# Kernel optimization log

Hardware: AMD Instinct MI355X
Metric: run time of the kernel (lower is better)

## Reference

```python
import jax, jax.numpy as jnp
import numpy as np

OUT = 7                # adaptive pool output size (7,7)
SPATIAL_SCALE = 1.0 / 16.0
NEG = jnp.float32(-3.0e38)  # acts as -inf for masked max


def setup_inputs() -> dict:
    key = jax.random.key(0)
    k1, k2, k3, k4, k5, k6 = jax.random.split(key, 6)
    B, C, H, W = 2, 256, 50, 50
    R = 256
    features = jax.random.normal(k1, (B, C, H, W), dtype=jnp.float32)
    # boxes in image coordinates (image = 800x800, stride 16)
    x1 = jax.random.uniform(k2, (R,), minval=0.0, maxval=500.0)
    y1 = jax.random.uniform(k3, (R,), minval=0.0, maxval=500.0)
    bw = jax.random.uniform(k4, (R,), minval=64.0, maxval=296.0)
    bh = jax.random.uniform(k5, (R,), minval=64.0, maxval=296.0)
    rois = jnp.stack([x1, y1, x1 + bw, y1 + bh], axis=1).astype(jnp.float32)  # [R,4]
    roi_indices = jax.random.randint(k6, (R,), 0, B, dtype=jnp.int64)
    return {"features": features, "rois": rois, "roi_indices": roi_indices}


def _roi_pool(features, rois, roi_indices):
    H, W = features.shape[2], features.shape[3]
    ri = (rois * SPATIAL_SCALE).astype(jnp.int32)           # truncation, as np.astype
    x1, y1, x2, y2 = ri[:, 0], ri[:, 1], ri[:, 2], ri[:, 3]
    # NOTE: original code slices features[idx, :, x1:x2, y1:y2] -> x indexes dim H, y indexes dim W
    Lh = x2 - x1                                            # [R]
    Lw = y2 - y1
    p = jnp.arange(OUT)
    # adaptive max pool bin boundaries (torch semantics): start=floor(i*L/OUT), end=ceil((i+1)*L/OUT)
    hstart = x1[:, None] + (p[None, :] * Lh[:, None]) // OUT                   # [R,OUT]
    hend = x1[:, None] + ((p[None, :] + 1) * Lh[:, None] + OUT - 1) // OUT
    wstart = y1[:, None] + (p[None, :] * Lw[:, None]) // OUT
    wend = y1[:, None] + ((p[None, :] + 1) * Lw[:, None] + OUT - 1) // OUT
    hidx = jnp.arange(H)
    widx = jnp.arange(W)
    row_mask = (hidx[None, None, :] >= hstart[:, :, None]) & (hidx[None, None, :] < hend[:, :, None])  # [R,OUT,H]
    col_mask = (widx[None, None, :] >= wstart[:, :, None]) & (widx[None, None, :] < wend[:, :, None])  # [R,OUT,W]

    feat = features[roi_indices]                            # [R,C,H,W]
    # reduce over W per output column (fixed small loop over OUT bins)
    cols = []
    for pw in range(OUT):
        m = col_mask[:, pw][:, None, None, :]               # [R,1,1,W]
        cols.append(jnp.max(jnp.where(m, feat, NEG), axis=3))  # [R,C,H]
    t = jnp.stack(cols, axis=-1)                            # [R,C,H,OUT]
    # reduce over H per output row
    rows = []
    for ph in range(OUT):
        m = row_mask[:, ph][:, None, :, None]               # [R,1,H,1]
        rows.append(jnp.max(jnp.where(m, t, NEG), axis=2))  # [R,C,OUT]
    return jnp.stack(rows, axis=2)                          # [R,C,OUT,OUT]


def reference(features, rois, roi_indices):
    return _roi_pool(features, rois, roi_indices)
```

## Files before the change

### kernel.cpp

```cpp
#include <hip/hip_runtime.h>
#include <cstddef>


namespace {
constexpr int OUTP = 7;
constexpr int CC = 256;
constexpr int HH = 50;
constexpr int WW = 50;
constexpr int HWSZ = HH * WW;
constexpr int CSPLIT = 8;
constexpr int CPS = CC / CSPLIT;
constexpr float NEGV = -3e38f;
constexpr int LMAX = 19;
constexpr int RSTR = 21;
constexpr int CSTR = LMAX * RSTR;
typedef float vf4 __attribute__((ext_vector_type(4), aligned(4)));
}

__global__ __launch_bounds__(256, 3) void roipool_fused(
    const float* __restrict__ feat, const float* __restrict__ rois,
    const int* __restrict__ ridx, float* __restrict__ out) {
    __shared__ float buf[CPS * CSTR];

    const int s = blockIdx.x;
    const int r = blockIdx.y;
    const int tid = threadIdx.x;

    const float4 rv = reinterpret_cast<const float4*>(rois)[r];
    int x1 = (int)(rv.x * 0.0625f);
    int y1 = (int)(rv.y * 0.0625f);
    int x2 = (int)(rv.z * 0.0625f);
    int y2 = (int)(rv.w * 0.0625f);
    int b = ridx[r];
    x1 = __builtin_amdgcn_readfirstlane(x1);
    y1 = __builtin_amdgcn_readfirstlane(y1);
    x2 = __builtin_amdgcn_readfirstlane(x2);
    y2 = __builtin_amdgcn_readfirstlane(y2);
    b = __builtin_amdgcn_readfirstlane(b);

    const int Lh = x2 - x1;
    const int Lw = y2 - y1;

    const float* fb = feat + (size_t)(b * CC + s * CPS) * HWSZ;
    float* obase = out + (size_t)(r * CC + s * CPS) * (OUTP * OUTP);

    const bool fast = (Lh >= 1 && Lh <= LMAX && Lw >= 1 && Lw <= LMAX &&
                       x1 >= 0 && y1 >= 0 && x2 < HH && y2 < WW);

    if (fast) {
        {
            const int c = tid >> 3;
            const int j = tid & 7;
            if (j < 5) {
                const float* gp = fb + (size_t)c * HWSZ + (size_t)x1 * WW + y1 + j * 4;
                float* lp = buf + c * CSTR + j * 4;
                for (int row = 0; row < Lh; ++row) {
                    const vf4 v = *reinterpret_cast<const vf4*>(gp + row * WW);
                    float* q = lp + row * RSTR;
                    q[0] = v.x;
                    q[1] = v.y;
                    q[2] = v.z;
                    q[3] = v.w;
                }
            }
        }
        __syncthreads();

        const int cc = tid & 31;
        const int q = tid >> 5;
        const float* cb = buf + cc * CSTR;
        float* ob = obase + (size_t)cc * (OUTP * OUTP);

#pragma unroll
        for (int k = 0; k < 7; ++k) {
            const int bin = q + k * 8;
            if (bin < 49) {
                const int ph = bin / OUTP;
                const int pw = bin - ph * OUTP;
                const int h0 = (ph * Lh) / OUTP;
                const int nh = ((ph + 1) * Lh + OUTP - 1) / OUTP - h0;
                const int w0 = (pw * Lw) / OUTP;
                const int nw = ((pw + 1) * Lw + OUTP - 1) / OUTP - w0;
                const float* wb = cb + h0 * RSTR + w0;
                float m = NEGV;
#pragma unroll
                for (int i = 0; i < 4; ++i) {
                    const int ro = (i < nh ? i : nh - 1) * RSTR;
#pragma unroll
                    for (int jj = 0; jj < 4; ++jj) {
                        const int co = (jj < nw ? jj : nw - 1);
                        m = fmaxf(m, wb[ro + co]);
                    }
                }
                __builtin_nontemporal_store(m, ob + bin);
            }
        }
    } else {
        const int cc = tid & 31;
        const int q = tid >> 5;
        const float* cb = fb + (size_t)cc * HWSZ;
        float* ob = obase + (size_t)cc * (OUTP * OUTP);

        for (int k = 0; k < 7; ++k) {
            const int bin = q + k * 8;
            if (bin < 49) {
                const int ph = bin / OUTP;
                const int pw = bin - ph * OUTP;
                int hs = x1 + (ph * Lh) / OUTP;
                int he = x1 + ((ph + 1) * Lh + OUTP - 1) / OUTP;
                int ws = y1 + (pw * Lw) / OUTP;
                int we = y1 + ((pw + 1) * Lw + OUTP - 1) / OUTP;
                hs = hs < 0 ? 0 : hs;
                he = he > HH ? HH : he;
                ws = ws < 0 ? 0 : ws;
                we = we > WW ? WW : we;
                float m = NEGV;
                for (int h = hs; h < he; ++h) {
                    for (int w = ws; w < we; ++w) {
                        m = fmaxf(m, cb[h * WW + w]);
                    }
                }
                ob[bin] = m;
            }
        }
    }
}

extern "C" void kernel_launch(void* const* d_in, const int* in_sizes, int n_in,
                              void* d_out, int out_size, void* d_ws, size_t ws_size,
                              hipStream_t stream) {
    const float* features = (const float*)d_in[0];
    const float* rois = (const float*)d_in[1];
    const int* ridx = (const int*)d_in[2];
    float* out = (float*)d_out;
    const int R = in_sizes[1] / 4;

    roipool_fused<<<dim3(CSPLIT, R), 256, 0, stream>>>(features, rois, ridx, out);
}
```

Baseline: 24.01 us.

## Split channels finer and stage ROI via aligned float2 loads spread over all threads

Doubles the channel split so each block handles 16 channels, giving twice as many blocks. The shared-memory staging loop is rewritten so all 256 threads cooperatively load aligned float2 segments across channel, row and column, instead of 5 of every 8 threads looping over rows with unaligned float4 loads. The row stride and compute mapping are adjusted to match, with a shift handling odd start columns. This aims to raise memory-level parallelism and reduce the serial per-row load latency, at the cost of more index arithmetic and smaller per-block work.

New measurement: 24.65 us. +2.6%, slower.

```diff
diff --git a/kernel.cpp b/kernel.cpp
--- a/kernel.cpp
+++ b/kernel.cpp
@@ -8,16 +8,19 @@
 constexpr int HH = 50;
 constexpr int WW = 50;
 constexpr int HWSZ = HH * WW;
-constexpr int CSPLIT = 8;
+constexpr int CSPLIT = 16;
 constexpr int CPS = CC / CSPLIT;
 constexpr float NEGV = -3e38f;
 constexpr int LMAX = 19;
-constexpr int RSTR = 21;
+constexpr int JSEG = 11;
+constexpr int RSTR = 23;
 constexpr int CSTR = LMAX * RSTR;
-typedef float vf4 __attribute__((ext_vector_type(4), aligned(4)));
+constexpr int NSEG_MAX = CPS * LMAX * JSEG;
+constexpr int KITER = (NSEG_MAX + 255) / 256;
+typedef float vf2 __attribute__((ext_vector_type(2)));
 }
 
-__global__ __launch_bounds__(256, 3) void roipool_fused(
+__global__ __launch_bounds__(256) void roipool_fused(
     const float* __restrict__ feat, const float* __restrict__ rois,
     const int* __restrict__ ridx, float* __restrict__ out) {
     __shared__ float buf[CPS * CSTR];
@@ -48,32 +51,36 @@
                        x1 >= 0 && y1 >= 0 && x2 < HH && y2 < WW);
 
     if (fast) {
-        {
-            const int c = tid >> 3;
-            const int j = tid & 7;
-            if (j < 5) {
-                const float* gp = fb + (size_t)c * HWSZ + (size_t)x1 * WW + y1 + j * 4;
-                float* lp = buf + c * CSTR + j * 4;
-                for (int row = 0; row < Lh; ++row) {
-                    const vf4 v = *reinterpret_cast<const vf4*>(gp + row * WW);
-                    float* q = lp + row * RSTR;
-                    q[0] = v.x;
-                    q[1] = v.y;
-                    q[2] = v.z;
-                    q[3] = v.w;
-                }
+        const int y1a = y1 & ~1;
+        const int shift = y1 & 1;
+        const int nseg = CPS * JSEG * Lh;
+        const float* gb = fb + (size_t)x1 * WW + y1a;
+
+#pragma unroll
+        for (int k = 0; k < KITER; ++k) {
+            const int seg = tid + k * 256;
+            if (seg < nseg) {
+                const int c = seg & (CPS - 1);
+                const int rj = seg >> 4;
+                const int j = rj % JSEG;
+                const int row = rj / JSEG;
+                const vf2 v = *reinterpret_cast<const vf2*>(
+                    gb + (size_t)c * HWSZ + row * WW + j * 2);
+                float* q = buf + c * CSTR + row * RSTR + j * 2;
+                q[0] = v.x;
+                q[1] = v.y;
             }
         }
         __syncthreads();
 
-        const int cc = tid & 31;
-        const int q = tid >> 5;
-        const float* cb = buf + cc * CSTR;
+        const int cc = tid & (CPS - 1);
+        const int qq = tid >> 4;
+        const float* cb = buf + cc * CSTR + shift;
         float* ob = obase + (size_t)cc * (OUTP * OUTP);
 
 #pragma unroll
-        for (int k = 0; k < 7; ++k) {
-            const int bin = q + k * 8;
+        for (int k = 0; k < 4; ++k) {
+            const int bin = qq + k * 16;
             if (bin < 49) {
                 const int ph = bin / OUTP;
                 const int pw = bin - ph * OUTP;
@@ -96,13 +103,13 @@
             }
         }
     } else {
-        const int cc = tid & 31;
-        const int q = tid >> 5;
+        const int cc = tid & (CPS - 1);
+        const int qq = tid >> 4;
         const float* cb = fb + (size_t)cc * HWSZ;
         float* ob = obase + (size_t)cc * (OUTP * OUTP);
 
-        for (int k = 0; k < 7; ++k) {
-            const int bin = q + k * 8;
+        for (int k = 0; k < 4; ++k) {
+            const int bin = qq + k * 16;
             if (bin < 49) {
                 const int ph = bin / OUTP;
                 const int pw = bin - ph * OUTP;
```
